# Kernel optimization log

Measured on AMD Instinct MI355X. Metric: run time of the kernel, lower is better.

## Reference

```python
import jax, jax.numpy as jnp
import numpy as np

N, E, D, H, C = 100000, 1600000, 64, 8, 10
NEG_SLOPE = 0.2


def setup_inputs() -> dict:
    key = jax.random.key(0)
    ks = jax.random.split(key, 20)
    rn = lambda k, sh: jax.random.normal(k, sh, jnp.float32) * 0.1
    return dict(
        x=jax.random.normal(ks[0], (N, D), jnp.float32),
        edge_index=jax.random.randint(ks[1], (2, E), 0, N),
        gcnK_W=rn(ks[2], (D, D)), gcnK_b=rn(ks[3], (D,)),
        gcnV_W=rn(ks[4], (D, D)), gcnV_b=rn(ks[5], (D,)),
        super_Q=rn(ks[6], (C, D)),
        mha_in_w=rn(ks[7], (3 * D, D)), mha_in_b=rn(ks[8], (3 * D,)),
        mha_out_w=rn(ks[9], (D, D)), mha_out_b=rn(ks[10], (D,)),
        gat_W=rn(ks[11], (D, D)), gat_Wc=rn(ks[12], (D, D)),
        gat_a_src=rn(ks[13], (D,)), gat_a_dst=rn(ks[14], (D,)),
        gat_b=rn(ks[15], (D,)),
        t1_W=rn(ks[16], (D, 2 * D)), t1_b=rn(ks[17], (2 * D,)),
        t2_W=rn(ks[18], (2 * D, D)), t2_b=rn(ks[19], (D,)),
    )


def _gcn(x, W, b, src, dst, norm_e):
    # PyG GCNConv: symmetric-normalized aggregation over (A + I)
    h = x @ W  # [N, D]
    agg = jax.ops.segment_sum(h[src] * norm_e[:, None], dst, num_segments=N)
    return agg + b


def _mha(q, k, v, in_w, in_b, out_w, out_b):
    # torch.nn.MultiheadAttention (unbatched), eval mode (dropout off)
    L, n, hd = q.shape[0], k.shape[0], D // H
    Wq, Wk, Wv = jnp.split(in_w, 3, axis=0)
    bq, bk, bv = jnp.split(in_b, 3)
    scale = 1.0 / float(np.sqrt(hd))
    qh = ((q @ Wq.T + bq) * scale).reshape(L, H, hd).transpose(1, 0, 2)  # [H,L,hd]
    kh = (k @ Wk.T + bk).reshape(n, H, hd).transpose(1, 0, 2)            # [H,n,hd]
    vh = (v @ Wv.T + bv).reshape(n, H, hd).transpose(1, 0, 2)
    attn = jax.nn.softmax(jnp.einsum('hld,hnd->hln', qh, kh), axis=-1)
    o = jnp.einsum('hln,hnd->hld', attn, vh).transpose(1, 0, 2).reshape(L, D)
    return o @ out_w.T + out_b


def _context_gat(x, src, dst, context, W, Wc, a_src, a_dst, b):
    # context-conditioned GAT: per-edge logits use node terms + global context gate
    h = x @ W
    c = context @ Wc  # [D]
    s_src = h @ (a_src + c)  # context modulates source attention vector
    s_dst = h @ a_dst
    logits = jax.nn.leaky_relu(s_src[src] + s_dst[dst], NEG_SLOPE)  # [E]
    m = jax.ops.segment_max(logits, dst, num_segments=N)
    ex = jnp.exp(logits - m[dst])
    denom = jax.ops.segment_sum(ex, dst, num_segments=N)
    alpha = ex / (denom[dst] + 1e-16)
    out = jax.ops.segment_sum(alpha[:, None] * h[src], dst, num_segments=N)
    return out + b


def reference(x, edge_index, gcnK_W, gcnK_b, gcnV_W, gcnV_b, super_Q,
              mha_in_w, mha_in_b, mha_out_w, mha_out_b,
              gat_W, gat_Wc, gat_a_src, gat_a_dst, gat_b,
              t1_W, t1_b, t2_W, t2_b):
    src, dst = edge_index[0], edge_index[1]
    loop = jnp.arange(N)
    srcl = jnp.concatenate([src, loop])
    dstl = jnp.concatenate([dst, loop])
    deg = jax.ops.segment_sum(jnp.ones_like(srcl, jnp.float32), dstl, num_segments=N)
    dinv = jnp.where(deg > 0, 1.0 / jnp.sqrt(deg), 0.0)
    norm_e = dinv[srcl] * dinv[dstl]
    x_K = _gcn(x, gcnK_W, gcnK_b, srcl, dstl, norm_e)
    x_V = _gcn(x, gcnV_W, gcnV_b, srcl, dstl, norm_e)
    cluster = _mha(super_Q, x_K, x_V, mha_in_w, mha_in_b, mha_out_w, mha_out_b)  # [C, D]
    context = jnp.mean(cluster, axis=0)  # [D]
    g = _context_gat(x_V, src, dst, context, gat_W, gat_Wc, gat_a_src, gat_a_dst, gat_b)
    h1 = jax.nn.relu(g @ t1_W + t1_b)
    return jax.nn.relu(h1 @ t2_W + t2_b)
```

## Files before the change

### kernel.cpp

```cpp
#include <hip/hip_runtime.h>
#include <hip/hip_bf16.h>
#include <stdint.h>

#define NN 100000
#define EE 1600000
#define NBK 391
#define CHUNK 4096
#define NCB 98
#define NPROJ 1563
#define NS 32

#define FMA4(xi, vv, a, base)                      \
  a[(base)+0] = fmaf((xi), (vv).x, a[(base)+0]);   \
  a[(base)+1] = fmaf((xi), (vv).y, a[(base)+1]);   \
  a[(base)+2] = fmaf((xi), (vv).z, a[(base)+2]);   \
  a[(base)+3] = fmaf((xi), (vv).w, a[(base)+3]);

__device__ inline unsigned pack_bf2(float a, float b) {
  __hip_bfloat162 t;
  t.x = __float2bfloat16(a);
  t.y = __float2bfloat16(b);
  return *reinterpret_cast<unsigned*>(&t);
}

__launch_bounds__(256)
__global__ void k_hist(const int* __restrict__ ei, int* __restrict__ histmat) {
  __shared__ int hist[NCB];
  int t = threadIdx.x;
  if (t < NCB) hist[t] = 0;
  __syncthreads();
  int base = blockIdx.x * CHUNK;
  int nb = EE - base; if (nb > CHUNK) nb = CHUNK;
  for (int k = t; k < nb; k += 256)
    atomicAdd(&hist[ei[EE + base + k] >> 10], 1);
  __syncthreads();
  if (t < NCB) histmat[blockIdx.x * NCB + t] = hist[t];
}

__launch_bounds__(256)
__global__ void k_sumcb(const int* __restrict__ histmat, int* __restrict__ cbsum) {
  __shared__ int red[4];
  int cb = blockIdx.x, t = threadIdx.x;
  int s = 0;
  for (int blk = t; blk < NBK; blk += 256) s += histmat[blk * NCB + cb];
#pragma unroll
  for (int off = 32; off > 0; off >>= 1) s += __shfl_down(s, off);
  if ((t & 63) == 0) red[t >> 6] = s;
  __syncthreads();
  if (t == 0) cbsum[cb] = red[0] + red[1] + red[2] + red[3];
}

__launch_bounds__(512)
__global__ void k_ppos(const int* __restrict__ histmat, const int* __restrict__ cbsum,
                       int* __restrict__ bstart, int* __restrict__ offsets,
                       int* __restrict__ ppos) {
  __shared__ int sm[512];
  __shared__ int sb[128];
  int cb = blockIdx.x, t = threadIdx.x;
  if (t < 128) sb[t] = (t < NCB) ? cbsum[t] : 0;
  __syncthreads();
  for (int off = 1; off < 128; off <<= 1) {
    int x = (t < 128 && t >= off) ? sb[t - off] : 0;
    __syncthreads();
    if (t < 128) sb[t] += x;
    __syncthreads();
  }
  int bs = (cb == 0) ? 0 : sb[cb - 1];
  if (t == 0) bstart[cb] = bs;
  if (cb == 0 && t == 0) { bstart[NCB] = EE; offsets[NN] = EE; }
  int v = (t < NBK) ? histmat[t * NCB + cb] : 0;
  sm[t] = v;
  __syncthreads();
  for (int off = 1; off < 512; off <<= 1) {
    int x = (t >= off) ? sm[t - off] : 0;
    __syncthreads();
    sm[t] += x;
    __syncthreads();
  }
  if (t < NBK) ppos[cb * NBK + t] = bs + sm[t] - v;
}

__launch_bounds__(256)
__global__ void k_fill_b(const int* __restrict__ ei, const int* __restrict__ ppos,
                         unsigned* __restrict__ brec) {
  __shared__ int hist[NCB], binstart[NCB], bincur[NCB], pbase[NCB];
  __shared__ unsigned lbuf[CHUNK];
  __shared__ unsigned char cbArr[CHUNK];
  int t = threadIdx.x;
  int base = blockIdx.x * CHUNK;
  int nb = EE - base; if (nb > CHUNK) nb = CHUNK;
  if (t < NCB) { hist[t] = 0; pbase[t] = ppos[t * NBK + blockIdx.x]; }
  __syncthreads();
  unsigned rec[16]; int rcb[16]; int cnt = 0;
  for (int k = t; k < nb; k += 256) {
    int s = ei[base + k], d = ei[EE + base + k];
    rec[cnt] = (unsigned)s | ((unsigned)(d & 1023) << 17);
    rcb[cnt] = d >> 10;
    atomicAdd(&hist[rcb[cnt]], 1);
    cnt++;
  }
  __syncthreads();
  if (t < NCB) binstart[t] = hist[t];
  __syncthreads();
  for (int off = 1; off < NCB; off <<= 1) {
    int v = (t < NCB && t >= off) ? binstart[t - off] : 0;
    __syncthreads();
    if (t < NCB) binstart[t] += v;
    __syncthreads();
  }
  if (t < NCB) { binstart[t] -= hist[t]; bincur[t] = 0; }
  __syncthreads();
  for (int i = 0; i < cnt; i++) {
    int c = rcb[i];
    int pos = atomicAdd(&bincur[c], 1);
    int p = binstart[c] + pos;
    lbuf[p] = rec[i];
    cbArr[p] = (unsigned char)c;
  }
  __syncthreads();
  for (int i = t; i < nb; i += 256) {
    int c = cbArr[i];
    brec[pbase[c] + (i - binstart[c])] = lbuf[i];
  }
}

__launch_bounds__(1024)
__global__ void k_fill_c(const unsigned* __restrict__ brec, const int* __restrict__ bstart,
                         int* __restrict__ csr, int* __restrict__ offsets,
                         float* __restrict__ dinv) {
  __shared__ int cnt[1024], sm[1024];
  int cbk = blockIdx.x, t = threadIdx.x;
  int nb0 = cbk << 10;
  int nn = NN - nb0; if (nn > 1024) nn = 1024;
  cnt[t] = 0;
  __syncthreads();
  int e0 = bstart[cbk], e1 = bstart[cbk + 1];
  for (int j = e0 + t; j < e1; j += 1024)
    atomicAdd(&cnt[brec[j] >> 17], 1);
  __syncthreads();
  int cv = cnt[t];
  sm[t] = cv;
  __syncthreads();
  for (int off = 1; off < 1024; off <<= 1) {
    int v = (t >= off) ? sm[t - off] : 0;
    __syncthreads();
    sm[t] += v;
    __syncthreads();
  }
  sm[t] -= cv;
  if (t < nn) {
    offsets[nb0 + t] = e0 + sm[t];
    dinv[nb0 + t] = rsqrtf((float)(cv + 1));
  }
  cnt[t] = 0;
  __syncthreads();
  for (int j = e0 + t; j < e1; j += 1024) {
    unsigned r = brec[j];
    int dl = r >> 17;
    int p = atomicAdd(&cnt[dl], 1);
    csr[e0 + sm[dl] + p] = r & 0x1FFFF;
  }
}

__global__ void k_prep(const float* __restrict__ x, const float* __restrict__ dinv,
                       unsigned* __restrict__ xbf2) {
  int i = blockIdx.x * 256 + threadIdx.x;
  if (i >= NN * 32) return;
  float dv = dinv[i >> 5];
  float2 v = ((const float2*)x)[i];
  xbf2[i] = pack_bf2(v.x * dv, v.y * dv);
}

__launch_bounds__(256)
__global__ void k_agg_x(const unsigned* __restrict__ xbf2, const int* __restrict__ offsets,
                        const int* __restrict__ csr, const float* __restrict__ dinv,
                        unsigned* __restrict__ axb) {
  int gid = blockIdx.x * 256 + threadIdx.x;
  int n = gid >> 6;
  if (n >= NN) return;
  int lane = gid & 63, q = lane & 7, grp = lane >> 3;
  int e0 = offsets[n], e1 = offsets[n + 1];
  float dv = dinv[n];
  float a[8];
#pragma unroll
  for (int i = 0; i < 8; i++) a[i] = 0.f;
  if (grp == 0) {
    uint4 u = ((const uint4*)(xbf2 + (size_t)n * 32))[q];
    unsigned uu[4] = {u.x, u.y, u.z, u.w};
#pragma unroll
    for (int p = 0; p < 4; p++) {
      __hip_bfloat162 v = *reinterpret_cast<__hip_bfloat162*>(&uu[p]);
      a[2 * p] += __bfloat162float(v.x);
      a[2 * p + 1] += __bfloat162float(v.y);
    }
  }
  int b2 = e0;
  for (; b2 + 8 < e1; b2 += 16) {
    int j0 = b2 + grp, j1 = j0 + 8;
    int s0 = csr[j0];
    bool ok1 = j1 < e1;
    int s1 = ok1 ? csr[j1] : s0;
    uint4 u0 = ((const uint4*)(xbf2 + (size_t)s0 * 32))[q];
    uint4 u1 = ((const uint4*)(xbf2 + (size_t)s1 * 32))[q];
    unsigned w0[4] = {u0.x, u0.y, u0.z, u0.w};
    unsigned w1[4] = {u1.x, u1.y, u1.z, u1.w};
#pragma unroll
    for (int p = 0; p < 4; p++) {
      __hip_bfloat162 v = *reinterpret_cast<__hip_bfloat162*>(&w0[p]);
      a[2 * p] += __bfloat162float(v.x);
      a[2 * p + 1] += __bfloat162float(v.y);
    }
    if (ok1) {
#pragma unroll
      for (int p = 0; p < 4; p++) {
        __hip_bfloat162 v = *reinterpret_cast<__hip_bfloat162*>(&w1[p]);
        a[2 * p] += __bfloat162float(v.x);
        a[2 * p + 1] += __bfloat162float(v.y);
      }
    }
  }
  for (; b2 < e1; b2 += 8) {
    int j = b2 + grp;
    if (j < e1) {
      int s = csr[j];
      uint4 u = ((const uint4*)(xbf2 + (size_t)s * 32))[q];
      unsigned uu[4] = {u.x, u.y, u.z, u.w};
#pragma unroll
      for (int p = 0; p < 4; p++) {
        __hip_bfloat162 v = *reinterpret_cast<__hip_bfloat162*>(&uu[p]);
        a[2 * p] += __bfloat162float(v.x);
        a[2 * p + 1] += __bfloat162float(v.y);
      }
    }
  }
#pragma unroll
  for (int i = 0; i < 8; i++) {
    a[i] += __shfl_xor(a[i], 8);
    a[i] += __shfl_xor(a[i], 16);
    a[i] += __shfl_xor(a[i], 32);
  }
  if (lane < 8) {
    uint4 u;
    u.x = pack_bf2(a[0] * dv, a[1] * dv);
    u.y = pack_bf2(a[2] * dv, a[3] * dv);
    u.z = pack_bf2(a[4] * dv, a[5] * dv);
    u.w = pack_bf2(a[6] * dv, a[7] * dv);
    ((uint4*)(axb + (size_t)n * 32))[q] = u;
  }
}

__global__ void k_fusew(const float* __restrict__ gcnK_W, const float* __restrict__ gcnK_b,
                        const float* __restrict__ gcnV_W, const float* __restrict__ gcnV_b,
                        const float* __restrict__ mha_in_w, const float* __restrict__ mha_in_b,
                        const float* __restrict__ gat_W, const float* __restrict__ sQ,
                        float* __restrict__ Wfk, float* __restrict__ Wfv,
                        float* __restrict__ Wfg, float* __restrict__ bf,
                        float* __restrict__ qh) {
  int blk = blockIdx.x;
  if (blk < 48) {
    int m = blk >> 4;
    int e = (blk & 15) * 256 + threadIdx.x;
    int i = e >> 6, c = e & 63;
    float s = 0.f;
    if (m == 0) {
      for (int j = 0; j < 64; j++) s = fmaf(gcnK_W[i * 64 + j], mha_in_w[(64 + c) * 64 + j], s);
      Wfk[e] = s;
    } else if (m == 1) {
      for (int j = 0; j < 64; j++) s = fmaf(gcnV_W[i * 64 + j], mha_in_w[(128 + c) * 64 + j], s);
      Wfv[e] = s;
    } else {
      for (int j = 0; j < 64; j++) s = fmaf(gcnV_W[i * 64 + j], gat_W[j * 64 + c], s);
      Wfg[e] = s;
    }
  } else if (blk == 48) {
    int t = threadIdx.x;
    if (t < 64) {
      float s = mha_in_b[64 + t];
      for (int j = 0; j < 64; j++) s = fmaf(gcnK_b[j], mha_in_w[(64 + t) * 64 + j], s);
      bf[t] = s;
    } else if (t < 128) {
      int c = t - 64;
      float s = mha_in_b[128 + c];
      for (int j = 0; j < 64; j++) s = fmaf(gcnV_b[j], mha_in_w[(128 + c) * 64 + j], s);
      bf[64 + c] = s;
    } else if (t < 192) {
      int c = t - 128;
      float s = 0.f;
      for (int j = 0; j < 64; j++) s = fmaf(gcnV_b[j], gat_W[j * 64 + c], s);
      bf[128 + c] = s;
    }
  } else {
    int t = (blk - 49) * 256 + threadIdx.x;
    if (t < 640) {
      int l = t >> 6, c = t & 63;
      float acc = 0.f;
      for (int i = 0; i < 64; i++) acc = fmaf(sQ[l * 64 + i], mha_in_w[c * 64 + i], acc);
      qh[t] = (acc + mha_in_b[c]) * 0.35355339059327373f;
    }
  }
}

__launch_bounds__(256)
__global__ void k_proj(const unsigned* __restrict__ axb, const float* __restrict__ Wfk,
                       const float* __restrict__ Wfv, const float* __restrict__ Wfg,
                       const float* __restrict__ bf, const float* __restrict__ a_dst,
                       const float* __restrict__ qh,
                       unsigned* __restrict__ hGb, float* __restrict__ s_dstv,
                       float* __restrict__ part) {
  __shared__ float sX[64 * 65];
  __shared__ float sWk[4096], sWv[4096], sWg[4096];
  __shared__ float sB[192], sAd[64], sq[640];
  int t = threadIdx.x;
  int base = blockIdx.x * 64;
  for (int i = t; i < 4096; i += 256) { sWk[i] = Wfk[i]; sWv[i] = Wfv[i]; sWg[i] = Wfg[i]; }
  if (t < 192) sB[t] = bf[t];
  if (t < 64) sAd[t] = a_dst[t];
  for (int i = t; i < 640; i += 256) sq[i] = qh[i];
  for (int idx = t; idx < 64 * 8; idx += 256) {
    int rl = idx >> 3, c8 = idx & 7;
    int row = base + rl;
    uint4 u = (row < NN) ? ((const uint4*)(axb + (size_t)row * 32))[c8]
                         : make_uint4(0u, 0u, 0u, 0u);
    unsigned uu[4] = {u.x, u.y, u.z, u.w};
    float* dst = sX + rl * 65 + c8 * 8;
#pragma unroll
    for (int p = 0; p < 4; p++) {
      __hip_bfloat162 v = *reinterpret_cast<__hip_bfloat162*>(&uu[p]);
      dst[2 * p] = __bfloat162float(v.x);
      dst[2 * p + 1] = __bfloat162float(v.y);
    }
  }
  __syncthreads();
  int cg = t & 7, rg = t >> 3;
  int r0 = rg * 2;
  float aK[16], aV[16], aG[16];
#pragma unroll
  for (int i = 0; i < 16; i++) { aK[i] = 0.f; aV[i] = 0.f; aG[i] = 0.f; }
  const float4* Wk4 = (const float4*)sWk;
  const float4* Wv4 = (const float4*)sWv;
  const float4* Wg4 = (const float4*)sWg;
#pragma unroll 2
  for (int i = 0; i < 64; i++) {
    float x0 = sX[r0 * 65 + i];
    float x1 = sX[(r0 + 1) * 65 + i];
    float4 wk0 = Wk4[i * 16 + cg * 2], wk1 = Wk4[i * 16 + cg * 2 + 1];
    float4 wv0 = Wv4[i * 16 + cg * 2], wv1 = Wv4[i * 16 + cg * 2 + 1];
    float4 wg0 = Wg4[i * 16 + cg * 2], wg1 = Wg4[i * 16 + cg * 2 + 1];
    FMA4(x0, wk0, aK, 0); FMA4(x0, wk1, aK, 4);
    FMA4(x1, wk0, aK, 8); FMA4(x1, wk1, aK, 12);
    FMA4(x0, wv0, aV, 0); FMA4(x0, wv1, aV, 4);
    FMA4(x1, wv0, aV, 8); FMA4(x1, wv1, aV, 12);
    FMA4(x0, wg0, aG, 0); FMA4(x0, wg1, aG, 4);
    FMA4(x1, wg0, aG, 8); FMA4(x1, wg1, aG, 12);
  }
  float s[10], o[80];
#pragma unroll
  for (int l = 0; l < 10; l++) s[l] = 0.f;
#pragma unroll
  for (int i = 0; i < 80; i++) o[i] = 0.f;
  const float4* sq4 = (const float4*)sq;
#pragma unroll
  for (int r = 0; r < 2; r++) {
    int row = base + r0 + r;
    bool ok = row < NN;
    int off = r * 8;
    float kv[8], vv[8], hg[8];
    float sd = 0.f;
#pragma unroll
    for (int c = 0; c < 8; c++) {
      kv[c] = aK[off + c] + sB[cg * 8 + c];
      vv[c] = aV[off + c] + sB[64 + cg * 8 + c];
      hg[c] = aG[off + c] + sB[128 + cg * 8 + c];
      sd = fmaf(hg[c], sAd[cg * 8 + c], sd);
    }
    sd += __shfl_xor(sd, 1);
    sd += __shfl_xor(sd, 2);
    sd += __shfl_xor(sd, 4);
    if (ok) {
#pragma unroll
      for (int l = 0; l < 10; l++) {
        float4 q0 = sq4[l * 16 + cg * 2], q1 = sq4[l * 16 + cg * 2 + 1];
        float z = q0.x * kv[0] + q0.y * kv[1] + q0.z * kv[2] + q0.w * kv[3] +
                  q1.x * kv[4] + q1.y * kv[5] + q1.z * kv[6] + q1.w * kv[7];
        float w = __expf(z);
        s[l] += w;
#pragma unroll
        for (int c = 0; c < 8; c++) o[l * 8 + c] = fmaf(w, vv[c], o[l * 8 + c]);
      }
      uint4 u;
      u.x = pack_bf2(hg[0], hg[1]);
      u.y = pack_bf2(hg[2], hg[3]);
      u.z = pack_bf2(hg[4], hg[5]);
      u.w = pack_bf2(hg[6], hg[7]);
      ((uint4*)(hGb + (size_t)row * 32))[cg] = u;
      if (cg == 0) s_dstv[row] = sd;
    }
  }
#pragma unroll
  for (int l = 0; l < 10; l++) {
    s[l] += __shfl_xor(s[l], 8);
    s[l] += __shfl_xor(s[l], 16);
    s[l] += __shfl_xor(s[l], 32);
  }
#pragma unroll
  for (int i = 0; i < 80; i++) {
    o[i] += __shfl_xor(o[i], 8);
    o[i] += __shfl_xor(o[i], 16);
    o[i] += __shfl_xor(o[i], 32);
  }
  __syncthreads();
  float* scratch = sX;
  int lane = t & 63, wave = t >> 6;
  if (lane < 8) {
#pragma unroll
    for (int l = 0; l < 10; l++) scratch[wave * 720 + lane * 90 + l] = s[l];
#pragma unroll
    for (int i = 0; i < 80; i++) scratch[wave * 720 + lane * 90 + 10 + i] = o[i];
  }
  __syncthreads();
  for (int j = t; j < 720; j += 256) {
    float v = scratch[j] + scratch[720 + j] + scratch[1440 + j] + scratch[2160 + j];
    part[(size_t)blockIdx.x * 720 + j] = v;
  }
}

__launch_bounds__(256)
__global__ void k_mred1(const float* __restrict__ part, float* __restrict__ part2) {
  int blk = blockIdx.x, t = threadIdx.x;
  int per = (NPROJ + NS - 1) / NS;
  int b0 = blk * per, b1 = b0 + per; if (b1 > NPROJ) b1 = NPROJ;
  float v0 = 0.f, v1 = 0.f, v2 = 0.f;
  for (int b = b0; b < b1; b++) {
    const float* row = part + (size_t)b * 720;
    v0 += row[t];
    if (t + 256 < 720) v1 += row[t + 256];
    if (t + 512 < 720) v2 += row[t + 512];
  }
  part2[(size_t)blk * 720 + t] = v0;
  if (t + 256 < 720) part2[(size_t)blk * 720 + t + 256] = v1;
  if (t + 512 < 720) part2[(size_t)blk * 720 + t + 512] = v2;
}

__global__ void k_context(const float* __restrict__ part2, const float* __restrict__ out_w,
                          const float* __restrict__ out_b, const float* __restrict__ a_src,
                          const float* __restrict__ gat_Wc, float* __restrict__ aeff) {
  __shared__ float po[640], cl[640], ctx[64], ac[720];
  int t = threadIdx.x;
  for (int j = t; j < 720; j += 640) {
    float v = 0.f;
#pragma unroll
    for (int s = 0; s < NS; s++) v += part2[(size_t)s * 720 + j];
    int cg = j / 90, r = j % 90;
    ac[(r < 10) ? (cg * 10 + r) : (80 + cg * 80 + (r - 10))] = v;
  }
  __syncthreads();
  {
    int h = t / 80, r = t % 80, l = r >> 3, j = r & 7;
    po[l * 64 + h * 8 + j] = ac[80 + t] / ac[h * 10 + l];
  }
  __syncthreads();
  {
    int l = t >> 6, d = t & 63;
    float v = out_b[d];
    for (int c = 0; c < 64; c++) v = fmaf(po[l * 64 + c], out_w[d * 64 + c], v);
    cl[t] = v;
  }
  __syncthreads();
  if (t < 64) {
    float m = 0.f;
#pragma unroll
    for (int l = 0; l < 10; l++) m += cl[l * 64 + t];
    ctx[t] = m * 0.1f;
  }
  __syncthreads();
  if (t < 64) {
    float v = a_src[t];
    for (int i = 0; i < 64; i++) v = fmaf(ctx[i], gat_Wc[i * 64 + t], v);
    aeff[t] = v;
  }
}

__launch_bounds__(256)
__global__ void k_ssrc(const unsigned* __restrict__ hGb, const float* __restrict__ aeff,
                       float* __restrict__ s_src) {
  int gid = blockIdx.x * 256 + threadIdx.x;
  int n = gid >> 6, lane = gid & 63;
  if (n >= NN) return;
  const __hip_bfloat16* hp = (const __hip_bfloat16*)hGb;
  float v = __bfloat162float(hp[(size_t)n * 64 + lane]) * aeff[lane];
#pragma unroll
  for (int off = 32; off > 0; off >>= 1) v += __shfl_xor(v, off);
  if (lane == 0) s_src[n] = v;
}

__launch_bounds__(256)
__global__ void k_gat(const int* __restrict__ offsets, const int* __restrict__ csr,
                      const float* __restrict__ s_src, const float* __restrict__ s_dstv,
                      const unsigned* __restrict__ hGb, const float* __restrict__ gat_b,
                      unsigned* __restrict__ gb) {
  int gid = blockIdx.x * 256 + threadIdx.x;
  int n = gid >> 6;
  if (n >= NN) return;
  int lane = gid & 63, q = lane & 7, grp = lane >> 3;
  int e0 = offsets[n], e1 = offsets[n + 1];
  float sd = s_dstv[n];
  float den = 0.f;
  float a[8];
#pragma unroll
  for (int i = 0; i < 8; i++) a[i] = 0.f;
  int b2 = e0;
  for (; b2 + 8 < e1; b2 += 16) {
    int j0 = b2 + grp, j1 = j0 + 8;
    int s0 = csr[j0];
    bool ok1 = j1 < e1;
    int s1 = ok1 ? csr[j1] : s0;
    float z0 = s_src[s0] + sd;
    float z1 = s_src[s1] + sd;
    uint4 u0 = ((const uint4*)(hGb + (size_t)s0 * 32))[q];
    uint4 u1 = ((const uint4*)(hGb + (size_t)s1 * 32))[q];
    unsigned w0[4] = {u0.x, u0.y, u0.z, u0.w};
    unsigned w1[4] = {u1.x, u1.y, u1.z, u1.w};
    z0 = z0 > 0.f ? z0 : 0.2f * z0;
    float ex0 = __expf(z0);
    den += ex0;
#pragma unroll
    for (int p = 0; p < 4; p++) {
      __hip_bfloat162 v = *reinterpret_cast<__hip_bfloat162*>(&w0[p]);
      a[2 * p] = fmaf(ex0, __bfloat162float(v.x), a[2 * p]);
      a[2 * p + 1] = fmaf(ex0, __bfloat162float(v.y), a[2 * p + 1]);
    }
    if (ok1) {
      z1 = z1 > 0.f ? z1 : 0.2f * z1;
      float ex1 = __expf(z1);
      den += ex1;
#pragma unroll
      for (int p = 0; p < 4; p++) {
        __hip_bfloat162 v = *reinterpret_cast<__hip_bfloat162*>(&w1[p]);
        a[2 * p] = fmaf(ex1, __bfloat162float(v.x), a[2 * p]);
        a[2 * p + 1] = fmaf(ex1, __bfloat162float(v.y), a[2 * p + 1]);
      }
    }
  }
  for (; b2 < e1; b2 += 8) {
    int j = b2 + grp;
    if (j < e1) {
      int s = csr[j];
      float z = s_src[s] + sd;
      z = z > 0.f ? z : 0.2f * z;
      float ex = __expf(z);
      den += ex;
      uint4 u = ((const uint4*)(hGb + (size_t)s * 32))[q];
      unsigned uu[4] = {u.x, u.y, u.z, u.w};
#pragma unroll
      for (int p = 0; p < 4; p++) {
        __hip_bfloat162 v = *reinterpret_cast<__hip_bfloat162*>(&uu[p]);
        a[2 * p] = fmaf(ex, __bfloat162float(v.x), a[2 * p]);
        a[2 * p + 1] = fmaf(ex, __bfloat162float(v.y), a[2 * p + 1]);
      }
    }
  }
  den += __shfl_xor(den, 8);
  den += __shfl_xor(den, 16);
  den += __shfl_xor(den, 32);
#pragma unroll
  for (int i = 0; i < 8; i++) {
    a[i] += __shfl_xor(a[i], 8);
    a[i] += __shfl_xor(a[i], 16);
    a[i] += __shfl_xor(a[i], 32);
  }
  float inv = 1.f / (den + 1e-16f);
  if (lane < 8) {
    uint4 u;
    u.x = pack_bf2(a[0] * inv + gat_b[q * 8 + 0], a[1] * inv + gat_b[q * 8 + 1]);
    u.y = pack_bf2(a[2] * inv + gat_b[q * 8 + 2], a[3] * inv + gat_b[q * 8 + 3]);
    u.z = pack_bf2(a[4] * inv + gat_b[q * 8 + 4], a[5] * inv + gat_b[q * 8 + 5]);
    u.w = pack_bf2(a[6] * inv + gat_b[q * 8 + 6], a[7] * inv + gat_b[q * 8 + 7]);
    ((uint4*)(gb + (size_t)n * 32))[q] = u;
  }
}

__launch_bounds__(256)
__global__ void k_mlp1(const unsigned* __restrict__ gb, const float* __restrict__ W1,
                       const float* __restrict__ b1, unsigned* __restrict__ h1b) {
  __shared__ float sX[32 * 65];
  __shared__ float sW[64 * 128];
  __shared__ float sb[128];
  int t = threadIdx.x;
  int base = blockIdx.x * 32;
  for (int i = t; i < 8192; i += 256) sW[i] = W1[i];
  if (t < 128) sb[t] = b1[t];
  for (int idx = t; idx < 32 * 8; idx += 256) {
    int rl = idx >> 3, c8 = idx & 7;
    int row = base + rl;
    uint4 u = (row < NN) ? ((const uint4*)(gb + (size_t)row * 32))[c8]
                         : make_uint4(0u, 0u, 0u, 0u);
    unsigned uu[4] = {u.x, u.y, u.z, u.w};
    float* dst = sX + rl * 65 + c8 * 8;
#pragma unroll
    for (int p = 0; p < 4; p++) {
      __hip_bfloat162 v = *reinterpret_cast<__hip_bfloat162*>(&uu[p]);
      dst[2 * p] = __bfloat162float(v.x);
      dst[2 * p + 1] = __bfloat162float(v.y);
    }
  }
  __syncthreads();
  int cg = t & 15, rg = t >> 4;
  int r0 = rg * 2;
  float a0[8], a1[8];
#pragma unroll
  for (int i = 0; i < 8; i++) { a0[i] = 0.f; a1[i] = 0.f; }
  const float4* W4 = (const float4*)sW;
#pragma unroll 4
  for (int i = 0; i < 64; i++) {
    float x0 = sX[r0 * 65 + i];
    float x1 = sX[(r0 + 1) * 65 + i];
    float4 w0 = W4[i * 32 + cg * 2], w1 = W4[i * 32 + cg * 2 + 1];
    FMA4(x0, w0, a0, 0); FMA4(x0, w1, a0, 4);
    FMA4(x1, w0, a1, 0); FMA4(x1, w1, a1, 4);
  }
#pragma unroll
  for (int r = 0; r < 2; r++) {
    int row = base + r0 + r;
    if (row >= NN) continue;
    float* a = r ? a1 : a0;
    float h[8];
#pragma unroll
    for (int c = 0; c < 8; c++) h[c] = fmaxf(a[c] + sb[cg * 8 + c], 0.f);
    uint4 u;
    u.x = pack_bf2(h[0], h[1]);
    u.y = pack_bf2(h[2], h[3]);
    u.z = pack_bf2(h[4], h[5]);
    u.w = pack_bf2(h[6], h[7]);
    ((uint4*)(h1b + (size_t)row * 64))[cg] = u;
  }
}

__launch_bounds__(256)
__global__ void k_mlp2(const unsigned* __restrict__ h1b, const float* __restrict__ W2,
                       const float* __restrict__ b2, float* __restrict__ out) {
  __shared__ unsigned sH[64 * 65];
  __shared__ float sW[128 * 64];
  __shared__ float sb[64];
  int t = threadIdx.x;
  int base = blockIdx.x * 64;
  for (int i = t; i < 8192; i += 256) sW[i] = W2[i];
  if (t < 64) sb[t] = b2[t];
  for (int idx = t; idx < 64 * 16; idx += 256) {
    int rl = idx >> 4, c4 = idx & 15;
    int row = base + rl;
    uint4 v = (row < NN) ? ((const uint4*)h1b)[(size_t)row * 16 + c4]
                         : make_uint4(0u, 0u, 0u, 0u);
    sH[rl * 65 + 4 * c4 + 0] = v.x;
    sH[rl * 65 + 4 * c4 + 1] = v.y;
    sH[rl * 65 + 4 * c4 + 2] = v.z;
    sH[rl * 65 + 4 * c4 + 3] = v.w;
  }
  __syncthreads();
  int cg = t & 7, rg = t >> 3;
  int r0 = rg * 2;
  float a0[8], a1[8];
#pragma unroll
  for (int i = 0; i < 8; i++) { a0[i] = 0.f; a1[i] = 0.f; }
  const float4* W4 = (const float4*)sW;
#pragma unroll 2
  for (int kp = 0; kp < 64; kp++) {
    unsigned u0 = sH[r0 * 65 + kp];
    unsigned u1 = sH[(r0 + 1) * 65 + kp];
    float x0a = __uint_as_float(u0 << 16), x0b = __uint_as_float(u0 & 0xffff0000u);
    float x1a = __uint_as_float(u1 << 16), x1b = __uint_as_float(u1 & 0xffff0000u);
    int k0 = 2 * kp, k1 = 2 * kp + 1;
    float4 wa0 = W4[k0 * 16 + cg * 2], wa1 = W4[k0 * 16 + cg * 2 + 1];
    float4 wb0 = W4[k1 * 16 + cg * 2], wb1 = W4[k1 * 16 + cg * 2 + 1];
    FMA4(x0a, wa0, a0, 0); FMA4(x0a, wa1, a0, 4);
    FMA4(x0b, wb0, a0, 0); FMA4(x0b, wb1, a0, 4);
    FMA4(x1a, wa0, a1, 0); FMA4(x1a, wa1, a1, 4);
    FMA4(x1b, wb0, a1, 0); FMA4(x1b, wb1, a1, 4);
  }
#pragma unroll
  for (int r = 0; r < 2; r++) {
    int row = base + r0 + r;
    if (row >= NN) continue;
    float* a = r ? a1 : a0;
    float4* op = (float4*)(out + (size_t)row * 64 + cg * 8);
    op[0] = make_float4(fmaxf(a[0] + sb[cg * 8 + 0], 0.f), fmaxf(a[1] + sb[cg * 8 + 1], 0.f),
                        fmaxf(a[2] + sb[cg * 8 + 2], 0.f), fmaxf(a[3] + sb[cg * 8 + 3], 0.f));
    op[1] = make_float4(fmaxf(a[4] + sb[cg * 8 + 4], 0.f), fmaxf(a[5] + sb[cg * 8 + 5], 0.f),
                        fmaxf(a[6] + sb[cg * 8 + 6], 0.f), fmaxf(a[7] + sb[cg * 8 + 7], 0.f));
  }
}

extern "C" void kernel_launch(void* const* d_in, const int* in_sizes, int n_in,
                              void* d_out, int out_size, void* d_ws, size_t ws_size,
                              hipStream_t stream) {
  (void)in_sizes; (void)n_in; (void)out_size; (void)ws_size;
  const float* x        = (const float*)d_in[0];
  const int*   ei       = (const int*)d_in[1];
  const float* gcnK_W   = (const float*)d_in[2];
  const float* gcnK_b   = (const float*)d_in[3];
  const float* gcnV_W   = (const float*)d_in[4];
  const float* gcnV_b   = (const float*)d_in[5];
  const float* super_Q  = (const float*)d_in[6];
  const float* mha_in_w = (const float*)d_in[7];
  const float* mha_in_b = (const float*)d_in[8];
  const float* mha_out_w= (const float*)d_in[9];
  const float* mha_out_b= (const float*)d_in[10];
  const float* gat_W    = (const float*)d_in[11];
  const float* gat_Wc   = (const float*)d_in[12];
  const float* gat_a_src= (const float*)d_in[13];
  const float* gat_a_dst= (const float*)d_in[14];
  const float* gat_b    = (const float*)d_in[15];
  const float* t1_W     = (const float*)d_in[16];
  const float* t1_b     = (const float*)d_in[17];
  const float* t2_W     = (const float*)d_in[18];
  const float* t2_b     = (const float*)d_in[19];

  char* ws = (char*)d_ws;
  size_t cur = 0;
  auto alloc = [&](size_t bytes) -> char* {
    char* p = ws + cur;
    cur = (cur + bytes + 255) & ~(size_t)255;
    return p;
  };
  int*      histmat = (int*)alloc((size_t)NBK * NCB * 4);
  int*      cbsum   = (int*)alloc((size_t)NCB * 4);
  int*      ppos    = (int*)alloc((size_t)NCB * NBK * 4);
  int*      bstart  = (int*)alloc((size_t)(NCB + 1) * 4);
  int*      offsets = (int*)alloc((size_t)(NN + 1) * 4);
  float*    dinv    = (float*)alloc((size_t)NN * 4);
  int*      csr     = (int*)alloc((size_t)EE * 4);
  unsigned* brec    = (unsigned*)alloc((size_t)EE * 4);
  float*    Wfk     = (float*)alloc(4096 * 4);
  float*    Wfv     = (float*)alloc(4096 * 4);
  float*    Wfg     = (float*)alloc(4096 * 4);
  float*    bfuse   = (float*)alloc(192 * 4);
  float*    qh      = (float*)alloc(640 * 4);
  float*    aeff    = (float*)alloc(64 * 4);
  float*    part    = (float*)alloc((size_t)NPROJ * 720 * 4);
  float*    part2   = (float*)alloc((size_t)NS * 720 * 4);
  float*    s_src   = (float*)alloc((size_t)NN * 4);
  float*    s_dstv  = (float*)alloc((size_t)NN * 4);
  unsigned* xbf     = (unsigned*)alloc((size_t)NN * 128);
  unsigned* axb     = (unsigned*)alloc((size_t)NN * 128);
  unsigned* hGb     = (unsigned*)alloc((size_t)NN * 128);
  unsigned* gb      = (unsigned*)alloc((size_t)NN * 128);
  unsigned* h1b     = (unsigned*)alloc((size_t)NN * 64 * 4);
  float*    g       = (float*)d_out;

  k_hist<<<NBK, 256, 0, stream>>>(ei, histmat);
  k_sumcb<<<NCB, 256, 0, stream>>>(histmat, cbsum);
  k_ppos<<<NCB, 512, 0, stream>>>(histmat, cbsum, bstart, offsets, ppos);
  k_fill_b<<<NBK, 256, 0, stream>>>(ei, ppos, brec);
  k_fill_c<<<NCB, 1024, 0, stream>>>(brec, bstart, csr, offsets, dinv);
  k_prep<<<(NN * 32 + 255) / 256, 256, 0, stream>>>(x, dinv, xbf);
  k_agg_x<<<NN / 4, 256, 0, stream>>>(xbf, offsets, csr, dinv, axb);
  k_fusew<<<52, 256, 0, stream>>>(gcnK_W, gcnK_b, gcnV_W, gcnV_b, mha_in_w, mha_in_b,
                                  gat_W, super_Q, Wfk, Wfv, Wfg, bfuse, qh);
  k_proj<<<NPROJ, 256, 0, stream>>>(axb, Wfk, Wfv, Wfg, bfuse, gat_a_dst, qh,
                                    hGb, s_dstv, part);
  k_mred1<<<NS, 256, 0, stream>>>(part, part2);
  k_context<<<1, 640, 0, stream>>>(part2, mha_out_w, mha_out_b, gat_a_src, gat_Wc, aeff);
  k_ssrc<<<NN / 4, 256, 0, stream>>>(hGb, aeff, s_src);
  k_gat<<<NN / 4, 256, 0, stream>>>(offsets, csr, s_src, s_dstv, hGb, gat_b, gb);
  k_mlp1<<<(NN + 31) / 32, 256, 0, stream>>>(gb, t1_W, t1_b, h1b);
  k_mlp2<<<(NN + 63) / 64, 256, 0, stream>>>(h1b, t2_W, t2_b, g);
}
```

Before: 438.8 us.

## Fold query into key weights and compute projections with bf16 MFMA

Precomputes one combined bf16 weight matrix of 208 columns: the V projection, the GAT projection, and attention logits with the scaled query folded into the K weights. The per-node projection then runs as 16x16x32 bf16 MFMA tiles, one 16-row tile per wave, instead of scalar FP32 FMAs against LDS-staged weights. Attention logits come straight out of the matmul, which removes the separate K projection and the per-query dot products. The fused weights are now bf16 rather than fp32, which costs some precision.

```diff
diff --git a/kernel.cpp b/kernel.cpp
--- a/kernel.cpp
+++ b/kernel.cpp
@@ -15,6 +15,10 @@
   a[(base)+1] = fmaf((xi), (vv).y, a[(base)+1]);   \
   a[(base)+2] = fmaf((xi), (vv).z, a[(base)+2]);   \
   a[(base)+3] = fmaf((xi), (vv).w, a[(base)+3]);
+
+typedef __attribute__((ext_vector_type(8))) short bf16x8;
+typedef __attribute__((ext_vector_type(4))) float f32x4;
+union FragU { uint4 u; bf16x8 h; };
 
 __device__ inline unsigned pack_bf2(float a, float b) {
   __hip_bfloat162 t;
@@ -253,173 +257,179 @@
                         const float* __restrict__ gcnV_W, const float* __restrict__ gcnV_b,
                         const float* __restrict__ mha_in_w, const float* __restrict__ mha_in_b,
                         const float* __restrict__ gat_W, const float* __restrict__ sQ,
-                        float* __restrict__ Wfk, float* __restrict__ Wfv,
-                        float* __restrict__ Wfg, float* __restrict__ bf,
-                        float* __restrict__ qh) {
-  int blk = blockIdx.x;
-  if (blk < 48) {
-    int m = blk >> 4;
-    int e = (blk & 15) * 256 + threadIdx.x;
-    int i = e >> 6, c = e & 63;
-    float s = 0.f;
-    if (m == 0) {
-      for (int j = 0; j < 64; j++) s = fmaf(gcnK_W[i * 64 + j], mha_in_w[(64 + c) * 64 + j], s);
-      Wfk[e] = s;
-    } else if (m == 1) {
-      for (int j = 0; j < 64; j++) s = fmaf(gcnV_W[i * 64 + j], mha_in_w[(128 + c) * 64 + j], s);
-      Wfv[e] = s;
-    } else {
-      for (int j = 0; j < 64; j++) s = fmaf(gcnV_W[i * 64 + j], gat_W[j * 64 + c], s);
-      Wfg[e] = s;
-    }
-  } else if (blk == 48) {
-    int t = threadIdx.x;
-    if (t < 64) {
-      float s = mha_in_b[64 + t];
-      for (int j = 0; j < 64; j++) s = fmaf(gcnK_b[j], mha_in_w[(64 + t) * 64 + j], s);
-      bf[t] = s;
-    } else if (t < 128) {
-      int c = t - 64;
-      float s = mha_in_b[128 + c];
-      for (int j = 0; j < 64; j++) s = fmaf(gcnV_b[j], mha_in_w[(128 + c) * 64 + j], s);
-      bf[64 + c] = s;
-    } else if (t < 192) {
-      int c = t - 128;
+                        unsigned* __restrict__ Wt, float* __restrict__ bb) {
+  int blk = blockIdx.x, t = threadIdx.x;
+  const float scale = 0.35355339059327373f;
+  if (blk < 26) {
+    int idx = blk * 256 + t;
+    int d = idx >> 5, kp = idx & 31;
+    float v2[2];
+#pragma unroll
+    for (int u2 = 0; u2 < 2; u2++) {
+      int k = kp * 2 + u2;
       float s = 0.f;
-      for (int j = 0; j < 64; j++) s = fmaf(gcnV_b[j], gat_W[j * 64 + c], s);
-      bf[128 + c] = s;
-    }
+      if (d < 64) {
+        for (int j = 0; j < 64; j++) s = fmaf(gcnV_W[k * 64 + j], mha_in_w[(128 + d) * 64 + j], s);
+      } else if (d < 128) {
+        int c = d - 64;
+        for (int j = 0; j < 64; j++) s = fmaf(gcnV_W[k * 64 + j], gat_W[j * 64 + c], s);
+      } else {
+        int hl = d - 128, h = hl / 10, lv = hl % 10;
+        for (int c = 0; c < 8; c++) {
+          int cp = h * 8 + c;
+          float wfk = 0.f, qv = mha_in_b[cp];
+          for (int j = 0; j < 64; j++) wfk = fmaf(gcnK_W[k * 64 + j], mha_in_w[(64 + cp) * 64 + j], wfk);
+          for (int i = 0; i < 64; i++) qv = fmaf(sQ[lv * 64 + i], mha_in_w[cp * 64 + i], qv);
+          s = fmaf(wfk, qv * scale, s);
+        }
+      }
+      v2[u2] = s;
+    }
+    Wt[idx] = pack_bf2(v2[0], v2[1]);
   } else {
-    int t = (blk - 49) * 256 + threadIdx.x;
-    if (t < 640) {
-      int l = t >> 6, c = t & 63;
-      float acc = 0.f;
-      for (int i = 0; i < 64; i++) acc = fmaf(sQ[l * 64 + i], mha_in_w[c * 64 + i], acc);
-      qh[t] = (acc + mha_in_b[c]) * 0.35355339059327373f;
-    }
-  }
-}
-
-__launch_bounds__(256)
-__global__ void k_proj(const unsigned* __restrict__ axb, const float* __restrict__ Wfk,
-                       const float* __restrict__ Wfv, const float* __restrict__ Wfg,
-                       const float* __restrict__ bf, const float* __restrict__ a_dst,
-                       const float* __restrict__ qh,
+    if (t < 208) {
+      float s;
+      if (t < 64) {
+        s = mha_in_b[128 + t];
+        for (int j = 0; j < 64; j++) s = fmaf(gcnV_b[j], mha_in_w[(128 + t) * 64 + j], s);
+      } else if (t < 128) {
+        int c = t - 64;
+        s = 0.f;
+        for (int j = 0; j < 64; j++) s = fmaf(gcnV_b[j], gat_W[j * 64 + c], s);
+      } else {
+        int hl = t - 128, h = hl / 10, lv = hl % 10;
+        s = 0.f;
+        for (int c = 0; c < 8; c++) {
+          int cp = h * 8 + c;
+          float kb = mha_in_b[64 + cp], qv = mha_in_b[cp];
+          for (int j = 0; j < 64; j++) kb = fmaf(gcnK_b[j], mha_in_w[(64 + cp) * 64 + j], kb);
+          for (int i = 0; i < 64; i++) qv = fmaf(sQ[lv * 64 + i], mha_in_w[cp * 64 + i], qv);
+          s = fmaf(kb, qv * scale, s);
+        }
+      }
+      bb[t] = s;
+    }
+  }
+}
+
+__launch_bounds__(256)
+__global__ void k_proj(const unsigned* __restrict__ axb, const unsigned* __restrict__ Wt,
+                       const float* __restrict__ bb, const float* __restrict__ a_dst,
                        unsigned* __restrict__ hGb, float* __restrict__ s_dstv,
                        float* __restrict__ part) {
-  __shared__ float sX[64 * 65];
-  __shared__ float sWk[4096], sWv[4096], sWg[4096];
-  __shared__ float sB[192], sAd[64], sq[640];
+  __shared__ unsigned short hg_lds[4][16][72];
+  __shared__ float wT[4][80][24];
+  __shared__ float red[4][720];
   int t = threadIdx.x;
+  int wid = t >> 6, l = t & 63;
+  int l15 = l & 15, lg = l >> 4;
   int base = blockIdx.x * 64;
-  for (int i = t; i < 4096; i += 256) { sWk[i] = Wfk[i]; sWv[i] = Wfv[i]; sWg[i] = Wfg[i]; }
-  if (t < 192) sB[t] = bf[t];
-  if (t < 64) sAd[t] = a_dst[t];
-  for (int i = t; i < 640; i += 256) sq[i] = qh[i];
-  for (int idx = t; idx < 64 * 8; idx += 256) {
-    int rl = idx >> 3, c8 = idx & 7;
-    int row = base + rl;
-    uint4 u = (row < NN) ? ((const uint4*)(axb + (size_t)row * 32))[c8]
-                         : make_uint4(0u, 0u, 0u, 0u);
-    unsigned uu[4] = {u.x, u.y, u.z, u.w};
-    float* dst = sX + rl * 65 + c8 * 8;
-#pragma unroll
-    for (int p = 0; p < 4; p++) {
-      __hip_bfloat162 v = *reinterpret_cast<__hip_bfloat162*>(&uu[p]);
-      dst[2 * p] = __bfloat162float(v.x);
-      dst[2 * p + 1] = __bfloat162float(v.y);
-    }
-  }
-  __syncthreads();
-  int cg = t & 7, rg = t >> 3;
-  int r0 = rg * 2;
-  float aK[16], aV[16], aG[16];
-#pragma unroll
-  for (int i = 0; i < 16; i++) { aK[i] = 0.f; aV[i] = 0.f; aG[i] = 0.f; }
-  const float4* Wk4 = (const float4*)sWk;
-  const float4* Wv4 = (const float4*)sWv;
-  const float4* Wg4 = (const float4*)sWg;
-#pragma unroll 2
-  for (int i = 0; i < 64; i++) {
-    float x0 = sX[r0 * 65 + i];
-    float x1 = sX[(r0 + 1) * 65 + i];
-    float4 wk0 = Wk4[i * 16 + cg * 2], wk1 = Wk4[i * 16 + cg * 2 + 1];
-    float4 wv0 = Wv4[i * 16 + cg * 2], wv1 = Wv4[i * 16 + cg * 2 + 1];
-    float4 wg0 = Wg4[i * 16 + cg * 2], wg1 = Wg4[i * 16 + cg * 2 + 1];
-    FMA4(x0, wk0, aK, 0); FMA4(x0, wk1, aK, 4);
-    FMA4(x1, wk0, aK, 8); FMA4(x1, wk1, aK, 12);
-    FMA4(x0, wv0, aV, 0); FMA4(x0, wv1, aV, 4);
-    FMA4(x1, wv0, aV, 8); FMA4(x1, wv1, aV, 12);
-    FMA4(x0, wg0, aG, 0); FMA4(x0, wg1, aG, 4);
-    FMA4(x1, wg0, aG, 8); FMA4(x1, wg1, aG, 12);
-  }
-  float s[10], o[80];
-#pragma unroll
-  for (int l = 0; l < 10; l++) s[l] = 0.f;
-#pragma unroll
-  for (int i = 0; i < 80; i++) o[i] = 0.f;
-  const float4* sq4 = (const float4*)sq;
-#pragma unroll
-  for (int r = 0; r < 2; r++) {
-    int row = base + r0 + r;
-    bool ok = row < NN;
-    int off = r * 8;
-    float kv[8], vv[8], hg[8];
-    float sd = 0.f;
-#pragma unroll
-    for (int c = 0; c < 8; c++) {
-      kv[c] = aK[off + c] + sB[cg * 8 + c];
-      vv[c] = aV[off + c] + sB[64 + cg * 8 + c];
-      hg[c] = aG[off + c] + sB[128 + cg * 8 + c];
-      sd = fmaf(hg[c], sAd[cg * 8 + c], sd);
-    }
-    sd += __shfl_xor(sd, 1);
-    sd += __shfl_xor(sd, 2);
-    sd += __shfl_xor(sd, 4);
-    if (ok) {
-#pragma unroll
-      for (int l = 0; l < 10; l++) {
-        float4 q0 = sq4[l * 16 + cg * 2], q1 = sq4[l * 16 + cg * 2 + 1];
-        float z = q0.x * kv[0] + q0.y * kv[1] + q0.z * kv[2] + q0.w * kv[3] +
-                  q1.x * kv[4] + q1.y * kv[5] + q1.z * kv[6] + q1.w * kv[7];
-        float w = __expf(z);
-        s[l] += w;
-#pragma unroll
-        for (int c = 0; c < 8; c++) o[l * 8 + c] = fmaf(w, vv[c], o[l * 8 + c]);
-      }
-      uint4 u;
-      u.x = pack_bf2(hg[0], hg[1]);
-      u.y = pack_bf2(hg[2], hg[3]);
-      u.z = pack_bf2(hg[4], hg[5]);
-      u.w = pack_bf2(hg[6], hg[7]);
-      ((uint4*)(hGb + (size_t)row * 32))[cg] = u;
-      if (cg == 0) s_dstv[row] = sd;
-    }
-  }
-#pragma unroll
-  for (int l = 0; l < 10; l++) {
-    s[l] += __shfl_xor(s[l], 8);
-    s[l] += __shfl_xor(s[l], 16);
-    s[l] += __shfl_xor(s[l], 32);
-  }
-#pragma unroll
-  for (int i = 0; i < 80; i++) {
-    o[i] += __shfl_xor(o[i], 8);
-    o[i] += __shfl_xor(o[i], 16);
-    o[i] += __shfl_xor(o[i], 32);
-  }
-  __syncthreads();
-  float* scratch = sX;
-  int lane = t & 63, wave = t >> 6;
-  if (lane < 8) {
-#pragma unroll
-    for (int l = 0; l < 10; l++) scratch[wave * 720 + lane * 90 + l] = s[l];
-#pragma unroll
-    for (int i = 0; i < 80; i++) scratch[wave * 720 + lane * 90 + 10 + i] = o[i];
-  }
+  int rowbase = base + wid * 16;
+
+  FragU a0, a1;
+  {
+    int r = rowbase + l15;
+    if (r < NN) {
+      const uint4* p = (const uint4*)(axb + (size_t)r * 32);
+      a0.u = p[lg];
+      a1.u = p[4 + lg];
+    } else {
+      a0.u = make_uint4(0u, 0u, 0u, 0u);
+      a1.u = a0.u;
+    }
+  }
+  f32x4 acc[13];
+#pragma unroll
+  for (int ct = 0; ct < 13; ct++) acc[ct] = (f32x4){0.f, 0.f, 0.f, 0.f};
+#pragma unroll
+  for (int ct = 0; ct < 13; ct++) {
+    const uint4* wp = (const uint4*)(Wt + (size_t)(ct * 16 + l15) * 32);
+    FragU b0, b1;
+    b0.u = wp[lg];
+    b1.u = wp[4 + lg];
+    acc[ct] = __builtin_amdgcn_mfma_f32_16x16x32_bf16(a0.h, b0.h, acc[ct], 0, 0, 0);
+    acc[ct] = __builtin_amdgcn_mfma_f32_16x16x32_bf16(a1.h, b1.h, acc[ct], 0, 0, 0);
+  }
+
+  float sdp[4] = {0.f, 0.f, 0.f, 0.f};
+#pragma unroll
+  for (int gt = 0; gt < 4; gt++) {
+    int col = gt * 16 + l15;
+    float bias = bb[64 + col];
+    float ad = a_dst[col];
+#pragma unroll
+    for (int r = 0; r < 4; r++) {
+      float hg = acc[4 + gt][r] + bias;
+      sdp[r] = fmaf(hg, ad, sdp[r]);
+      hg_lds[wid][lg * 4 + r][col] = (unsigned short)(pack_bf2(hg, 0.f) & 0xffffu);
+    }
+  }
+#pragma unroll
+  for (int r = 0; r < 4; r++) {
+    float v = sdp[r];
+    v += __shfl_xor(v, 1); v += __shfl_xor(v, 2);
+    v += __shfl_xor(v, 4); v += __shfl_xor(v, 8);
+    int row = rowbase + lg * 4 + r;
+    if (l15 == 0 && row < NN) s_dstv[row] = v;
+  }
+  asm volatile("s_waitcnt lgkmcnt(0)" ::: "memory");
+#pragma unroll
+  for (int p2 = 0; p2 < 2; p2++) {
+    int cid = l + 64 * p2;
+    int rl = cid >> 3, c8 = cid & 7;
+    int row = rowbase + rl;
+    uint4 u = *(const uint4*)&hg_lds[wid][rl][c8 * 8];
+    if (row < NN) ((uint4*)(hGb + (size_t)row * 32))[c8] = u;
+  }
+
+#pragma unroll
+  for (int zt = 0; zt < 5; zt++) {
+    int zcol = zt * 16 + l15;
+    float bias = bb[128 + zcol];
+    float sp = 0.f;
+#pragma unroll
+    for (int r = 0; r < 4; r++) {
+      int row = rowbase + lg * 4 + r;
+      float z = acc[8 + zt][r] + bias;
+      float w = (row < NN) ? __expf(z) : 0.f;
+      wT[wid][zcol][lg * 4 + r] = w;
+      sp += w;
+    }
+    sp += __shfl_xor(sp, 16);
+    sp += __shfl_xor(sp, 32);
+    if (l < 16) {
+      int h = zcol / 10, lv = zcol % 10;
+      red[wid][h * 90 + lv] = sp;
+    }
+  }
+
+  asm volatile("s_waitcnt lgkmcnt(0)" ::: "memory");
+#pragma unroll
+  for (int vt = 0; vt < 4; vt++) {
+    int col = vt * 16 + l15;
+    float bias = bb[col];
+    int h = col >> 3;
+    float vv[4];
+#pragma unroll
+    for (int r = 0; r < 4; r++) vv[r] = acc[vt][r] + bias;
+    float oo[10];
+#pragma unroll
+    for (int lv = 0; lv < 10; lv++) {
+      const float4 w4 = *(const float4*)&wT[wid][h * 10 + lv][lg * 4];
+      oo[lv] = w4.x * vv[0] + w4.y * vv[1] + w4.z * vv[2] + w4.w * vv[3];
+    }
+#pragma unroll
+    for (int lv = 0; lv < 10; lv++) {
+      float v = oo[lv];
+      v += __shfl_xor(v, 16);
+      v += __shfl_xor(v, 32);
+      if (l < 16) red[wid][h * 90 + 10 + lv * 8 + (col & 7)] = v;
+    }
+  }
+
   __syncthreads();
   for (int j = t; j < 720; j += 256) {
-    float v = scratch[j] + scratch[720 + j] + scratch[1440 + j] + scratch[2160 + j];
+    float v = red[0][j] + red[1][j] + red[2][j] + red[3][j];
     part[(size_t)blockIdx.x * 720 + j] = v;
   }
 }
@@ -729,11 +739,8 @@
   float*    dinv    = (float*)alloc((size_t)NN * 4);
   int*      csr     = (int*)alloc((size_t)EE * 4);
   unsigned* brec    = (unsigned*)alloc((size_t)EE * 4);
-  float*    Wfk     = (float*)alloc(4096 * 4);
-  float*    Wfv     = (float*)alloc(4096 * 4);
-  float*    Wfg     = (float*)alloc(4096 * 4);
-  float*    bfuse   = (float*)alloc(192 * 4);
-  float*    qh      = (float*)alloc(640 * 4);
+  unsigned* Wt      = (unsigned*)alloc((size_t)208 * 32 * 4);
+  float*    bb      = (float*)alloc(208 * 4);
   float*    aeff    = (float*)alloc(64 * 4);
   float*    part    = (float*)alloc((size_t)NPROJ * 720 * 4);
   float*    part2   = (float*)alloc((size_t)NS * 720 * 4);
@@ -753,10 +760,9 @@
   k_fill_c<<<NCB, 1024, 0, stream>>>(brec, bstart, csr, offsets, dinv);
   k_prep<<<(NN * 32 + 255) / 256, 256, 0, stream>>>(x, dinv, xbf);
   k_agg_x<<<NN / 4, 256, 0, stream>>>(xbf, offsets, csr, dinv, axb);
-  k_fusew<<<52, 256, 0, stream>>>(gcnK_W, gcnK_b, gcnV_W, gcnV_b, mha_in_w, mha_in_b,
-                                  gat_W, super_Q, Wfk, Wfv, Wfg, bfuse, qh);
-  k_proj<<<NPROJ, 256, 0, stream>>>(axb, Wfk, Wfv, Wfg, bfuse, gat_a_dst, qh,
-                                    hGb, s_dstv, part);
+  k_fusew<<<27, 256, 0, stream>>>(gcnK_W, gcnK_b, gcnV_W, gcnV_b, mha_in_w, mha_in_b,
+                                  gat_W, super_Q, Wt, bb);
+  k_proj<<<NPROJ, 256, 0, stream>>>(axb, Wt, bb, gat_a_dst, hGb, s_dstv, part);
   k_mred1<<<NS, 256, 0, stream>>>(part, part2);
   k_context<<<1, 640, 0, stream>>>(part2, mha_out_w, mha_out_b, gat_a_src, gat_Wc, aeff);
   k_ssrc<<<NN / 4, 256, 0, stream>>>(hGb, aeff, s_src);
```

Result: slower. 459.8 us (+4.8%).
